# Kernel optimization log

Hardware: AMD Instinct MI355X
Metric: run time of the kernel (lower is better)

The kernel has to match this reference:

```python
import jax, jax.numpy as jnp
import numpy as np

N = 10000      # nodes
E = 320000     # edges (avg degree 32)
H = 64         # hidden_nf
D = 3          # num_dims
L = 4          # n_layers
IN_NODE = 1
IN_EDGE = 2
CEMB = 16      # class_embedding_dim
FH = 32        # field_hidden_size


def setup_inputs() -> dict:
    key = jax.random.key(0)
    ks = iter(jax.random.split(key, 64))
    def nrm(shape, scale=0.05):
        return jax.random.normal(next(ks), shape, dtype=jnp.float32) * scale
    def zeros(shape):
        return jnp.zeros(shape, dtype=jnp.float32)
    inp = {
        # forward args
        "h": nrm((N, IN_NODE), 1.0),
        "x": nrm((N, D), 1.0),
        "vel": nrm((N, D), 1.0),
        "edge_attr": nrm((E, IN_EDGE), 1.0),
        "edges": jax.random.randint(next(ks), (2, E), 0, N, dtype=jnp.int32),
        "charges": jax.random.randint(next(ks), (N,), 0, 2, dtype=jnp.int32),
        # node embedding Linear(in_node_nf, hidden_nf)
        "emb_W": nrm((IN_NODE, H)), "emb_b": zeros((H,)),
        # FieldNetwork: Embedding(2, 16) + MLP(2*D+16 -> 32 -> 32 -> D), SiLU
        "cls_emb": nrm((2, CEMB)),
        "f_W1": nrm((2 * D + CEMB, FH)), "f_b1": zeros((FH,)),
        "f_W2": nrm((FH, FH)), "f_b2": zeros((FH,)),
        "f_W3": nrm((FH, D)), "f_b3": zeros((D,)),
        # per-layer E_GCL_vel_field params, stacked on leading layer dim L
        # edge_mlp: (2H + 1 radial + in_edge_nf) -> H -> H, SiLU after both
        "e_W1": nrm((L, 2 * H + 1 + IN_EDGE, H)), "e_b1": zeros((L, H)),
        "e_W2": nrm((L, H, H)), "e_b2": zeros((L, H)),
        # node_mlp: (H + H) -> H -> H, SiLU only after first
        "n_W1": nrm((L, 2 * H, H)), "n_b1": zeros((L, H)),
        "n_W2": nrm((L, H, H)), "n_b2": zeros((L, H)),
        # coord_mlp: H -> H -> 1 (last layer bias-free, small xavier init)
        "c_W1": nrm((L, H, H)), "c_b1": zeros((L, H)),
        "c_W2": nrm((L, H, 1), 0.001),
        # coord_mlp_vel: H -> H -> 1
        "v_W1": nrm((L, H, H)), "v_b1": zeros((L, H)),
        "v_W2": nrm((L, H, 1)), "v_b2": zeros((L, 1)),
        # coord_mlp_field: H -> H -> 1 (field gating, Aether extension)
        "g_W1": nrm((L, H, H)), "g_b1": zeros((L, H)),
        "g_W2": nrm((L, H, 1)), "g_b2": zeros((L, 1)),
    }
    return inp


def _egnn_forward(h, x, vel, edge_attr, emb_W, emb_b, cls_emb,
                  f_W1, f_b1, f_W2, f_b2, f_W3, f_b3,
                  e_W1, e_b1, e_W2, e_b2, n_W1, n_b1, n_W2, n_b2,
                  c_W1, c_b1, c_W2, v_W1, v_b1, v_W2, v_b2,
                  g_W1, g_b1, g_W2, g_b2, edges, charges):
    row, col = edges[0], edges[1]
    # FieldNetwork: field(pos, vel, charge_class) -> [N, D]
    finp = jnp.concatenate([x, vel, cls_emb[charges]], axis=-1)   # [N, 2D+CEMB]
    fh = jax.nn.silu(finp @ f_W1 + f_b1)
    fh = jax.nn.silu(fh @ f_W2 + f_b2)
    field = fh @ f_W3 + f_b3                                       # [N, D]

    hh = h @ emb_W + emb_b                                         # [N, H]
    coord = x
    ones_e = jnp.ones((E, 1), dtype=x.dtype)
    for i in range(L):
        # coord2radial
        diff = coord[row] - coord[col]                             # [E, D]
        radial = jnp.sum(diff * diff, axis=-1, keepdims=True)      # [E, 1]
        # edge model (gather + MLP)
        e_in = jnp.concatenate([hh[row], hh[col], radial, edge_attr], axis=-1)
        m = jax.nn.silu(e_in @ e_W1[i] + e_b1[i])
        m = jax.nn.silu(m @ e_W2[i] + e_b2[i])                     # [E, H]
        # coord model: mean-aggregate weighted diffs (coords_weight = 1.0)
        cw = jax.nn.silu(m @ c_W1[i] + c_b1[i]) @ c_W2[i]          # [E, 1]
        trans = diff * cw
        csum = jax.ops.segment_sum(trans, row, num_segments=N)     # [N, D]
        cnt = jax.ops.segment_sum(ones_e, row, num_segments=N)     # [N, 1]
        coord = coord + csum / jnp.maximum(cnt, 1.0)
        # velocity and field terms
        vw = jax.nn.silu(hh @ v_W1[i] + v_b1[i]) @ v_W2[i] + v_b2[i]   # [N,1]
        gw = jax.nn.silu(hh @ g_W1[i] + g_b1[i]) @ g_W2[i] + g_b2[i]   # [N,1]
        coord = coord + vw * vel + gw * field
        # node model (scatter-sum messages + MLP)
        magg = jax.ops.segment_sum(m, row, num_segments=N)         # [N, H]
        n_in = jnp.concatenate([hh, magg], axis=-1)
        hh = jax.nn.silu(n_in @ n_W1[i] + n_b1[i]) @ n_W2[i] + n_b2[i]
    return coord


def reference(h, x, vel, edge_attr, edges, charges, emb_W, emb_b, cls_emb,
              f_W1, f_b1, f_W2, f_b2, f_W3, f_b3,
              e_W1, e_b1, e_W2, e_b2, n_W1, n_b1, n_W2, n_b2,
              c_W1, c_b1, c_W2, v_W1, v_b1, v_W2, v_b2,
              g_W1, g_b1, g_W2, g_b2):
    return _egnn_forward(h, x, vel, edge_attr, emb_W, emb_b, cls_emb,
                         f_W1, f_b1, f_W2, f_b2, f_W3, f_b3,
                         e_W1, e_b1, e_W2, e_b2, n_W1, n_b1, n_W2, n_b2,
                         c_W1, c_b1, c_W2, v_W1, v_b1, v_W2, v_b2,
                         g_W1, g_b1, g_W2, g_b2, edges, charges)
```

## Files before the change

kernel.cpp:

```cpp
#include <hip/hip_runtime.h>
#include <hip/hip_bf16.h>

typedef unsigned short ushort_t;
typedef unsigned int uint_t;

#define NN    10000
#define NE    320000
#define NL    4
#define EBLK  64
#define NEBLK 5000
#define NPB   64
#define NNODEBLK 157
#define NPB2  16
#define NODEBLK2 625

#define OFF_FIELD 0
#define OFF_HH    30000
#define OFF_CSUM  670000
#define OFF_MAGG  700000
#define IOFF_CNTI   0
#define IOFF_OFF    10000
#define IOFF_CURSOR 20001
#define IOFF_PERM   30001
#define IOFF_PRER   350004
#define IOFF_PREC   670004
#define IOFF_WCONV  990004
#define WC_EW1  0
#define WC_EW2  4096
#define WC_CW1  6144
#define WC_VW1  8192
#define WC_GW1  10240
#define WC_NW1  12288

__device__ __forceinline__ float silu(float x) {
    return x * __builtin_amdgcn_rcpf(1.0f + __expf(-x));
}

typedef __fp16 half2v __attribute__((ext_vector_type(2)));
typedef __fp16 f16x8 __attribute__((ext_vector_type(8)));
typedef float f32x4 __attribute__((ext_vector_type(4)));
union U4H8 { uint4 u; f16x8 h; };
__device__ __forceinline__ half2v u2h(uint_t u) {
    union { uint_t u; half2v h; } x; x.u = u; return x.h;
}
__device__ __forceinline__ uint_t h2u(half2v h) {
    union { half2v h; uint_t u; } x; x.h = h; return x.u;
}
__device__ __forceinline__ half2v pkrtz(float a, float b) {
    return __builtin_amdgcn_cvt_pkrtz(a, b);
}
__device__ __forceinline__ float dot2h(half2v a, uint_t w, float c) {
#if __has_builtin(__builtin_amdgcn_fdot2)
    return __builtin_amdgcn_fdot2(a, u2h(w), c, false);
#else
    union { uint_t u; __fp16 h[2]; } x; x.u = w;
    return c + (float)a.x * (float)x.h[0] + (float)a.y * (float)x.h[1];
#endif
}
__device__ __forceinline__ ushort_t f2hbits(float f) {
    union { __fp16 h; ushort_t u; } x; x.h = (__fp16)f; return x.u;
}

__global__ __launch_bounds__(256) void wconv_kernel(
    const float* __restrict__ eW1, const float* __restrict__ eW2,
    const float* __restrict__ cW1, const float* __restrict__ vW1,
    const float* __restrict__ gW1, const float* __restrict__ nW1,
    uint_t* __restrict__ out)
{
    const int l = blockIdx.x;
    const int t = threadIdx.x;
    uint_t* o = out + l * 16384;
    const float* e1 = eW1 + l * 8384;
    const float* e2 = eW2 + l * 4096;
    const float* c1 = cW1 + l * 4096;
    const float* v1 = vW1 + l * 4096;
    const float* g1 = gW1 + l * 4096;
    const float* n1 = nW1 + l * 8192;

    for (int i = t; i < 4096; i += 256)
        o[WC_EW1 + i] = h2u(pkrtz(e1[(i >> 6) * 128 + (i & 63)],
                                  e1[(i >> 6) * 128 + 64 + (i & 63)]));
    for (int i = t; i < 2048; i += 256) {
        const int kp = i >> 6, bc = i & 63;
        const uint_t v = h2u(pkrtz(e2[kp * 128 + bc], e2[kp * 128 + 64 + bc]));
        o[WC_EW2 + bc * 32 + (((kp >> 2) ^ (bc & 7)) << 2) + (kp & 3)] = v;
    }
    for (int i = t; i < 2048; i += 256) {
        const int kp = i >> 6, bc = i & 63;
        const uint_t v = h2u(pkrtz(c1[kp * 128 + bc], c1[kp * 128 + 64 + bc]));
        o[WC_CW1 + bc * 32 + (((kp >> 2) ^ (bc & 7)) << 2) + (kp & 3)] = v;
    }
    for (int i = t; i < 2048; i += 256)
        o[WC_VW1 + i] = h2u(pkrtz(v1[(i >> 6) * 128 + (i & 63)],
                                  v1[(i >> 6) * 128 + 64 + (i & 63)]));
    for (int i = t; i < 2048; i += 256)
        o[WC_GW1 + i] = h2u(pkrtz(g1[(i >> 6) * 128 + (i & 63)],
                                  g1[(i >> 6) * 128 + 64 + (i & 63)]));
    for (int i = t; i < 4096; i += 256)
        o[WC_NW1 + i] = h2u(pkrtz(n1[(i >> 6) * 128 + (i & 63)],
                                  n1[(i >> 6) * 128 + 64 + (i & 63)]));
}

__global__ __launch_bounds__(256) void counti_kernel(const int* __restrict__ rows,
                                                     int* __restrict__ cnti) {
    const int e = blockIdx.x * 256 + threadIdx.x;
    if (e < NE) {
        int r = rows[e];
        r = ((uint_t)r < (uint_t)NN) ? r : 0;
        atomicAdd(&cnti[r], 1);
    }
}

__global__ __launch_bounds__(1024) void scan_kernel(const int* __restrict__ cnti,
                                                    int* __restrict__ off,
                                                    int* __restrict__ cursor) {
    __shared__ int part[1024];
    const int t = threadIdx.x;
    const int base = t * 10;
    int loc[10];
    int s = 0;
    #pragma unroll
    for (int i = 0; i < 10; i++) {
        const int idx = base + i;
        const int v = (idx < NN) ? cnti[idx] : 0;
        loc[i] = s; s += v;
    }
    part[t] = s;
    __syncthreads();
    const int own = s;
    for (int d = 1; d < 1024; d <<= 1) {
        const int v = (t >= d) ? part[t - d] : 0;
        __syncthreads();
        part[t] += v;
        __syncthreads();
    }
    const int excl = part[t] - own;
    #pragma unroll
    for (int i = 0; i < 10; i++) {
        const int idx = base + i;
        if (idx < NN) { const int o = excl + loc[i]; off[idx] = o; cursor[idx] = o; }
    }
    if (t == 0) off[NN] = NE;
}

__global__ __launch_bounds__(256) void scatter_kernel(const int* __restrict__ rows,
                                                      int* __restrict__ cursor,
                                                      int* __restrict__ perm) {
    const int e = blockIdx.x * 256 + threadIdx.x;
    if (e < NE) {
        int r = rows[e];
        r = ((uint_t)r < (uint_t)NN) ? r : 0;
        const int pos = atomicAdd(&cursor[r], 1);
        if ((uint_t)pos < (uint_t)NE) perm[pos] = e;
    }
}

__global__ __launch_bounds__(256) void node_init(
    const float* __restrict__ hsrc, const float* __restrict__ xsrc,
    const float* __restrict__ vsrc, const int* __restrict__ charges,
    const float* __restrict__ cls,
    const float* __restrict__ fW1, const float* __restrict__ fb1,
    const float* __restrict__ fW2, const float* __restrict__ fb2,
    const float* __restrict__ fW3, const float* __restrict__ fb3,
    const float* __restrict__ embW, const float* __restrict__ embb,
    float* __restrict__ coord, float* __restrict__ field, float* __restrict__ hh)
{
    __shared__ float sFW1[704], sFW2[1024], sFW3[96];
    __shared__ float sFB1[32], sFB2[32], sFB3[3], sCLS[32], sEW[64], sEB[64];
    const int t = threadIdx.x;
    for (int i = t; i < 704; i += 256) sFW1[i] = fW1[i];
    for (int i = t; i < 1024; i += 256) sFW2[i] = fW2[i];
    if (t < 96) sFW3[t] = fW3[t];
    if (t < 32) { sFB1[t] = fb1[t]; sFB2[t] = fb2[t]; sCLS[t] = cls[t]; }
    if (t < 3)  sFB3[t] = fb3[t];
    if (t < 64) { sEW[t] = embW[t]; sEB[t] = embb[t]; }
    __syncthreads();

    const int n = blockIdx.x * 256 + t;
    if (n >= NN) return;

    float fin[22];
    #pragma unroll
    for (int d = 0; d < 3; d++) {
        fin[d]     = xsrc[3 * n + d];
        fin[3 + d] = vsrc[3 * n + d];
        coord[3 * n + d] = fin[d];
    }
    int ci = charges[n];
    ci = ((uint_t)ci < 2u) ? ci : 0;
    const int cix = ci * 16;
    #pragma unroll
    for (int k = 0; k < 16; k++) fin[6 + k] = sCLS[cix + k];

    float h1[32];
    #pragma unroll
    for (int j = 0; j < 32; j++) h1[j] = sFB1[j];
    #pragma unroll
    for (int k = 0; k < 22; k++) {
        const float v = fin[k];
        #pragma unroll
        for (int j = 0; j < 32; j++) h1[j] += v * sFW1[k * 32 + j];
    }
    #pragma unroll
    for (int j = 0; j < 32; j++) h1[j] = silu(h1[j]);

    float h2[32];
    #pragma unroll
    for (int j = 0; j < 32; j++) h2[j] = sFB2[j];
    #pragma unroll
    for (int k = 0; k < 32; k++) {
        const float v = h1[k];
        #pragma unroll
        for (int j = 0; j < 32; j++) h2[j] += v * sFW2[k * 32 + j];
    }
    #pragma unroll
    for (int j = 0; j < 32; j++) h2[j] = silu(h2[j]);

    #pragma unroll
    for (int d = 0; d < 3; d++) {
        float s = sFB3[d];
        #pragma unroll
        for (int j = 0; j < 32; j++) s += h2[j] * sFW3[j * 3 + d];
        field[3 * n + d] = s;
    }

    const float hv = hsrc[n];
    #pragma unroll
    for (int j = 0; j < 64; j++) hh[(size_t)n * 64 + j] = hv * sEW[j] + sEB[j];
}

__global__ __launch_bounds__(256, 4) void pre_kernel(
    const float* __restrict__ hh,
    const uint_t* __restrict__ w1p, const float* __restrict__ gEB1,
    uint_t* __restrict__ preR, uint_t* __restrict__ preC)
{
    __shared__ __align__(16) uint_t sW1p[4096];
    __shared__ float sB1[64];
    const int t = threadIdx.x;
    for (int i = t; i < 1024; i += 256)
        ((uint4*)sW1p)[i] = ((const uint4*)w1p)[i];
    if (t < 64) sB1[t] = gEB1[t];
    __syncthreads();

    const int ni = t >> 2, q = t & 3;
    int n = blockIdx.x * NPB + ni;
    const bool valid = (n < NN);
    n = valid ? n : (NN - 1);
    const float4* h4p = (const float4*)(hh + (size_t)n * 64);

    float acc[16];
    #pragma unroll
    for (int j = 0; j < 16; j++) acc[j] = sB1[q * 16 + j];
    #pragma unroll
    for (int kk = 0; kk < 16; kk++) {
        const float4 a = h4p[kk];
        const half2v p0 = pkrtz(a.x, a.y);
        const half2v p1 = pkrtz(a.z, a.w);
        const uint4* w0 = (const uint4*)&sW1p[(2 * kk) * 64 + q * 16];
        const uint4* w1 = (const uint4*)&sW1p[(2 * kk + 1) * 64 + q * 16];
        #pragma unroll
        for (int j4 = 0; j4 < 4; j4++) {
            const uint4 wa = w0[j4], wb = w1[j4];
            acc[4*j4+0] = dot2h(p1, wb.x, dot2h(p0, wa.x, acc[4*j4+0]));
            acc[4*j4+1] = dot2h(p1, wb.y, dot2h(p0, wa.y, acc[4*j4+1]));
            acc[4*j4+2] = dot2h(p1, wb.z, dot2h(p0, wa.z, acc[4*j4+2]));
            acc[4*j4+3] = dot2h(p1, wb.w, dot2h(p0, wa.w, acc[4*j4+3]));
        }
    }
    if (valid) {
        uint4 o0, o1;
        o0.x = h2u(pkrtz(acc[0],  acc[1]));  o0.y = h2u(pkrtz(acc[2],  acc[3]));
        o0.z = h2u(pkrtz(acc[4],  acc[5]));  o0.w = h2u(pkrtz(acc[6],  acc[7]));
        o1.x = h2u(pkrtz(acc[8],  acc[9]));  o1.y = h2u(pkrtz(acc[10], acc[11]));
        o1.z = h2u(pkrtz(acc[12], acc[13])); o1.w = h2u(pkrtz(acc[14], acc[15]));
        uint4* dst = (uint4*)(preR + (size_t)n * 32 + q * 8);
        dst[0] = o0; dst[1] = o1;
    }

    #pragma unroll
    for (int j = 0; j < 16; j++) acc[j] = 0.f;
    #pragma unroll
    for (int kk = 0; kk < 16; kk++) {
        const float4 a = h4p[kk];
        const half2v p0 = pkrtz(a.x, a.y);
        const half2v p1 = pkrtz(a.z, a.w);
        const uint4* w0 = (const uint4*)&sW1p[(32 + 2 * kk) * 64 + q * 16];
        const uint4* w1 = (const uint4*)&sW1p[(33 + 2 * kk) * 64 + q * 16];
        #pragma unroll
        for (int j4 = 0; j4 < 4; j4++) {
            const uint4 wa = w0[j4], wb = w1[j4];
            acc[4*j4+0] = dot2h(p1, wb.x, dot2h(p0, wa.x, acc[4*j4+0]));
            acc[4*j4+1] = dot2h(p1, wb.y, dot2h(p0, wa.y, acc[4*j4+1]));
            acc[4*j4+2] = dot2h(p1, wb.z, dot2h(p0, wa.z, acc[4*j4+2]));
            acc[4*j4+3] = dot2h(p1, wb.w, dot2h(p0, wa.w, acc[4*j4+3]));
        }
    }
    if (valid) {
        uint4 o0, o1;
        o0.x = h2u(pkrtz(acc[0],  acc[1]));  o0.y = h2u(pkrtz(acc[2],  acc[3]));
        o0.z = h2u(pkrtz(acc[4],  acc[5]));  o0.w = h2u(pkrtz(acc[6],  acc[7]));
        o1.x = h2u(pkrtz(acc[8],  acc[9]));  o1.y = h2u(pkrtz(acc[10], acc[11]));
        o1.z = h2u(pkrtz(acc[12], acc[13])); o1.w = h2u(pkrtz(acc[14], acc[15]));
        uint4* dst = (uint4*)(preC + (size_t)n * 32 + q * 8);
        dst[0] = o0; dst[1] = o1;
    }
}

__global__ __launch_bounds__(256, 8) void edge_kernel(
    const int* __restrict__ rows, const int* __restrict__ cols,
    const int* __restrict__ perm,
    const float* __restrict__ coord,
    const float* __restrict__ eattr,
    const float* __restrict__ gEW1,
    const uint_t* __restrict__ ewp,
    const float* __restrict__ gEB2,
    const float* __restrict__ gCB1, const float* __restrict__ gCW2,
    const uint_t* __restrict__ preR, const uint_t* __restrict__ preC,
    float* __restrict__ csum, float* __restrict__ magg)
{
    __shared__ __align__(16) uint_t tileh[EBLK * 32];
    __shared__ __align__(16) uint_t sWp[2048];
    __shared__ float sExtW[3 * 64];
    __shared__ float sB2[64], sCB1[64], sCW2v[64];
    __shared__ float scw[EBLK];
    __shared__ int   sr[EBLK], sc[EBLK], se[EBLK];
    __shared__ int   segstart[EBLK + 1];
    __shared__ int   snseg;

    const int t = threadIdx.x;
    const int bid = blockIdx.x;
    const int lb  = (bid & 7) * (NEBLK / 8) + (bid >> 3);

    const uint4 cwr0 = ((const uint4*)(ewp + WC_CW1))[t];
    const uint4 cwr1 = ((const uint4*)(ewp + WC_CW1))[t + 256];

    for (int i = t; i < 512; i += 256)
        ((uint4*)sWp)[i] = ((const uint4*)(ewp + WC_EW2))[i];
    if (t < 192) sExtW[t] = gEW1[8192 + t];
    if (t < 64) { sB2[t] = gEB2[t]; sCB1[t] = gCB1[t]; sCW2v[t] = gCW2[t]; }

    if (t < EBLK) {
        int e = perm[lb * EBLK + t];
        e = ((uint_t)e < (uint_t)NE) ? e : 0;
        int r = rows[e], c = cols[e];
        r = ((uint_t)r < (uint_t)NN) ? r : 0;
        c = ((uint_t)c < (uint_t)NN) ? c : 0;
        se[t] = e; sr[t] = r; sc[t] = c;
    }
    __syncthreads();

    if (t < EBLK) {
        const int flag = (t == 0) ? 1 : ((sr[t] != sr[t - 1]) ? 1 : 0);
        int isc = flag;
        #pragma unroll
        for (int d = 1; d < EBLK; d <<= 1) {
            const int up = __shfl_up(isc, d);
            if (t >= d) isc += up;
        }
        if (flag) segstart[isc - 1] = t;
        if (t == EBLK - 1) { snseg = isc; segstart[isc] = EBLK; }
    }
    __syncthreads();
    const int nseg = snseg;

    const int ei = t >> 2;
    const int q  = t & 3;
    const int e7 = ei & 7;
    const int r = sr[ei], c = sc[ei], e = se[ei];

    const float dx = coord[3 * r + 0] - coord[3 * c + 0];
    const float dy = coord[3 * r + 1] - coord[3 * c + 1];
    const float dz = coord[3 * r + 2] - coord[3 * c + 2];
    const float radial = dx * dx + dy * dy + dz * dz;
    const float2 ea = ((const float2*)eattr)[e];

    union { uint4 v[2]; uint_t a[8]; } R, C;
    {
        const uint4* pr = (const uint4*)(preR + (size_t)r * 32);
        const uint4* pc = (const uint4*)(preC + (size_t)c * 32);
        R.v[0] = pr[q * 2]; R.v[1] = pr[q * 2 + 1];
        C.v[0] = pc[q * 2]; C.v[1] = pc[q * 2 + 1];
    }
    float acc16[16];
    #pragma unroll
    for (int p = 0; p < 8; p++) {
        const half2v hr = u2h(R.a[p]);
        const half2v hc = u2h(C.a[p]);
        acc16[2 * p]     = (float)hr.x + (float)hc.x;
        acc16[2 * p + 1] = (float)hr.y + (float)hc.y;
    }
    {
        const float ext3[3] = {radial, ea.x, ea.y};
        #pragma unroll
        for (int x = 0; x < 3; x++) {
            const float v = ext3[x];
            const float* w = &sExtW[x * 64 + q * 16];
            #pragma unroll
            for (int j = 0; j < 16; j++) acc16[j] += v * w[j];
        }
    }
    #pragma unroll
    for (int j = 0; j < 16; j++) acc16[j] = silu(acc16[j]);
    {
        uint4 g0, g1;
        g0.x = h2u(pkrtz(acc16[0],  acc16[1]));  g0.y = h2u(pkrtz(acc16[2],  acc16[3]));
        g0.z = h2u(pkrtz(acc16[4],  acc16[5]));  g0.w = h2u(pkrtz(acc16[6],  acc16[7]));
        g1.x = h2u(pkrtz(acc16[8],  acc16[9]));  g1.y = h2u(pkrtz(acc16[10], acc16[11]));
        g1.z = h2u(pkrtz(acc16[12], acc16[13])); g1.w = h2u(pkrtz(acc16[14], acc16[15]));
        ((uint4*)tileh)[ei * 8 + ((q * 2) ^ e7)]     = g0;
        ((uint4*)tileh)[ei * 8 + ((q * 2 + 1) ^ e7)] = g1;
    }
    __syncthreads();

    const int lane = t & 63;
    const int wv   = t >> 6;
    const int lrow = lane & 15;
    const int lkg  = lane >> 4;
    const int arow = wv * 16 + lrow;
    const int e7a  = arow & 7;

    U4H8 a0, a1;
    a0.u = ((const uint4*)tileh)[arow * 8 + (lkg ^ e7a)];
    a1.u = ((const uint4*)tileh)[arow * 8 + ((4 + lkg) ^ e7a)];

    f32x4 accn[4];
    #pragma unroll
    for (int n = 0; n < 4; n++) {
        const float b = sB2[n * 16 + lrow];
        f32x4 v = {b, b, b, b};
        accn[n] = v;
    }
    #pragma unroll
    for (int n = 0; n < 4; n++) {
        const int bc = n * 16 + lrow;
        const int b7 = bc & 7;
        U4H8 b0, b1;
        b0.u = ((const uint4*)sWp)[bc * 8 + (lkg ^ b7)];
        b1.u = ((const uint4*)sWp)[bc * 8 + ((4 + lkg) ^ b7)];
        accn[n] = __builtin_amdgcn_mfma_f32_16x16x32_f16(a0.h, b0.h, accn[n], 0, 0, 0);
        accn[n] = __builtin_amdgcn_mfma_f32_16x16x32_f16(a1.h, b1.h, accn[n], 0, 0, 0);
    }
    __syncthreads();

    ((uint4*)sWp)[t]       = cwr0;
    ((uint4*)sWp)[t + 256] = cwr1;
    {
        ushort_t* th16 = (ushort_t*)tileh;
        const int mrow = wv * 16 + lkg * 4;
        #pragma unroll
        for (int n = 0; n < 4; n++) {
            const int ch = n * 16 + lrow;
            const int wi = ch >> 1;
            const int wg = wi >> 2, wj = wi & 3, hl = ch & 1;
            #pragma unroll
            for (int r2 = 0; r2 < 4; r2++) {
                const int edge = mrow + r2;
                th16[(edge * 32 + ((wg ^ (edge & 7)) << 2) + wj) * 2 + hl] =
                    f2hbits(silu(accn[n][r2]));
            }
        }
    }
    __syncthreads();

    U4H8 ma0, ma1;
    ma0.u = ((const uint4*)tileh)[arow * 8 + (lkg ^ e7a)];
    ma1.u = ((const uint4*)tileh)[arow * 8 + ((4 + lkg) ^ e7a)];
    f32x4 cacc[4];
    #pragma unroll
    for (int n = 0; n < 4; n++) {
        const float b = sCB1[n * 16 + lrow];
        f32x4 v = {b, b, b, b};
        cacc[n] = v;
    }
    #pragma unroll
    for (int n = 0; n < 4; n++) {
        const int bc = n * 16 + lrow;
        const int b7 = bc & 7;
        U4H8 b0, b1;
        b0.u = ((const uint4*)sWp)[bc * 8 + (lkg ^ b7)];
        b1.u = ((const uint4*)sWp)[bc * 8 + ((4 + lkg) ^ b7)];
        cacc[n] = __builtin_amdgcn_mfma_f32_16x16x32_f16(ma0.h, b0.h, cacc[n], 0, 0, 0);
        cacc[n] = __builtin_amdgcn_mfma_f32_16x16x32_f16(ma1.h, b1.h, cacc[n], 0, 0, 0);
    }
    float p0 = 0.f, p1 = 0.f, p2 = 0.f, p3 = 0.f;
    #pragma unroll
    for (int n = 0; n < 4; n++) {
        const float w2v = sCW2v[n * 16 + lrow];
        p0 += silu(cacc[n][0]) * w2v;
        p1 += silu(cacc[n][1]) * w2v;
        p2 += silu(cacc[n][2]) * w2v;
        p3 += silu(cacc[n][3]) * w2v;
    }
    #pragma unroll
    for (int m = 1; m <= 8; m <<= 1) {
        p0 += __shfl_xor(p0, m);
        p1 += __shfl_xor(p1, m);
        p2 += __shfl_xor(p2, m);
        p3 += __shfl_xor(p3, m);
    }
    if (lrow == 0) {
        const int mrow = wv * 16 + lkg * 4;
        scw[mrow + 0] = p0; scw[mrow + 1] = p1;
        scw[mrow + 2] = p2; scw[mrow + 3] = p3;
    }

    for (int w = t; w < nseg * 64; w += 256) {
        const int lr2 = w >> 6, cc = w & 63;
        const int pp0 = segstart[lr2], pp1 = segstart[lr2 + 1];
        const int kp = cc >> 1, hi = cc & 1;
        const int kg = kp >> 2, kj = kp & 3;
        float s = 0.f;
        for (int p = pp0; p < pp1; p++) {
            const half2v h = u2h(tileh[p * 32 + ((kg ^ (p & 7)) << 2) + kj]);
            s += hi ? (float)h.y : (float)h.x;
        }
        atomicAdd(&magg[(size_t)sr[pp0] * 64 + cc], s);
    }
    __syncthreads();

    const float cw = scw[ei];
    float* tf = (float*)tileh;
    if (q < 3) tf[ei * 4 + q] = (q == 0 ? dx : (q == 1 ? dy : dz)) * cw;
    __syncthreads();
    for (int w = t; w < nseg * 3; w += 256) {
        const int lr2 = w / 3, cc = w - 3 * lr2;
        const int pp0 = segstart[lr2], pp1 = segstart[lr2 + 1];
        float s = 0.f;
        for (int p = pp0; p < pp1; p++) s += tf[p * 4 + cc];
        atomicAdd(&csum[3 * sr[pp0] + cc], s);
    }
}

__global__ __launch_bounds__(256, 2) void node_kernel(
    const uint_t* __restrict__ nwp,
    const uint_t* __restrict__ nwpn,
    const float* __restrict__ gVB1, const float* __restrict__ gVW2,
    const float* __restrict__ gVB2,
    const float* __restrict__ gGB1, const float* __restrict__ gGW2,
    const float* __restrict__ gGB2,
    const float* __restrict__ gNB1,
    const float* __restrict__ gNW2, const float* __restrict__ gNB2,
    const float* __restrict__ gB1n,
    float* __restrict__ csum, const int* __restrict__ off,
    const float* __restrict__ vsrc, const float* __restrict__ field,
    float* __restrict__ magg,
    float* __restrict__ coord, float* __restrict__ hh,
    uint_t* __restrict__ preR, uint_t* __restrict__ preC, const int emit_pre)
{
    __shared__ __align__(16) uint_t sNW1p[4096];
    __shared__ __align__(16) uint_t sW1np[4096];
    __shared__ __align__(16) uint_t sVW1p[2048];
    __shared__ __align__(16) uint_t sGW1p[2048];
    __shared__ __align__(16) float sNW2[4096];
    __shared__ __align__(16) float tile[NPB2 * 136];
    __shared__ float sNB1[64], sNB2[64], sB1n[64];

    const int t = threadIdx.x;
    for (int i = t; i < 1024; i += 256)
        ((uint4*)sNW1p)[i] = ((const uint4*)(nwp + WC_NW1))[i];
    for (int i = t; i < 1024; i += 256)
        ((uint4*)sW1np)[i] = ((const uint4*)(nwpn + WC_EW1))[i];
    for (int i = t; i < 512; i += 256)
        ((uint4*)sVW1p)[i] = ((const uint4*)(nwp + WC_VW1))[i];
    for (int i = t; i < 512; i += 256)
        ((uint4*)sGW1p)[i] = ((const uint4*)(nwp + WC_GW1))[i];
    for (int i = t; i < 1024; i += 256)
        ((float4*)sNW2)[i] = ((const float4*)gNW2)[i];
    if (t < 64) { sNB1[t] = gNB1[t]; sNB2[t] = gNB2[t]; sB1n[t] = gB1n[t]; }

    const int ni = t >> 4;
    const int q  = t & 15;
    const int n = blockIdx.x * NPB2 + ni;
    float* T = &tile[ni * 136];

    ((float4*)T)[q]        = ((const float4*)(hh + (size_t)n * 64))[q];
    ((float4*)(T + 68))[q] = ((const float4*)(magg + (size_t)n * 64))[q];
    __syncthreads();

    float v4[4], g4[4];
    {
        const float4 bv = ((const float4*)gVB1)[q];
        const float4 bg = ((const float4*)gGB1)[q];
        v4[0] = bv.x; v4[1] = bv.y; v4[2] = bv.z; v4[3] = bv.w;
        g4[0] = bg.x; g4[1] = bg.y; g4[2] = bg.z; g4[3] = bg.w;
    }
    #pragma unroll 8
    for (int kp = 0; kp < 32; kp++) {
        const half2v p = pkrtz(T[2 * kp], T[2 * kp + 1]);
        const uint4 wv = *(const uint4*)&sVW1p[kp * 64 + q * 4];
        const uint4 wg = *(const uint4*)&sGW1p[kp * 64 + q * 4];
        v4[0] = dot2h(p, wv.x, v4[0]); v4[1] = dot2h(p, wv.y, v4[1]);
        v4[2] = dot2h(p, wv.z, v4[2]); v4[3] = dot2h(p, wv.w, v4[3]);
        g4[0] = dot2h(p, wg.x, g4[0]); g4[1] = dot2h(p, wg.y, g4[1]);
        g4[2] = dot2h(p, wg.z, g4[2]); g4[3] = dot2h(p, wg.w, g4[3]);
    }
    float partv, partg;
    {
        const float4 wv2 = ((const float4*)gVW2)[q];
        const float4 wg2 = ((const float4*)gGW2)[q];
        partv = silu(v4[0]) * wv2.x + silu(v4[1]) * wv2.y
              + silu(v4[2]) * wv2.z + silu(v4[3]) * wv2.w;
        partg = silu(g4[0]) * wg2.x + silu(g4[1]) * wg2.y
              + silu(g4[2]) * wg2.z + silu(g4[3]) * wg2.w;
    }
    partv += __shfl_xor(partv, 1);  partg += __shfl_xor(partg, 1);
    partv += __shfl_xor(partv, 2);  partg += __shfl_xor(partg, 2);
    partv += __shfl_xor(partv, 4);  partg += __shfl_xor(partg, 4);
    partv += __shfl_xor(partv, 8);  partg += __shfl_xor(partg, 8);
    const float vw = partv + gVB2[0];
    const float gw = partg + gGB2[0];

    if (q == 0) {
        const float cn = fmaxf((float)(off[n + 1] - off[n]), 1.0f);
        #pragma unroll
        for (int d = 0; d < 3; d++)
            coord[3 * n + d] += csum[3 * n + d] / cn
                              + vw * vsrc[3 * n + d]
                              + gw * field[3 * n + d];
    }

    float aA[4], aB[4];
    {
        const float4 b = ((const float4*)sNB1)[q];
        aA[0] = b.x; aA[1] = b.y; aA[2] = b.z; aA[3] = b.w;
        aB[0] = aB[1] = aB[2] = aB[3] = 0.f;
    }
    #pragma unroll 8
    for (int kp = 0; kp < 32; kp++) {
        const half2v pA = pkrtz(T[2 * kp], T[2 * kp + 1]);
        const half2v pB = pkrtz(T[68 + 2 * kp], T[68 + 2 * kp + 1]);
        const uint4 wA = *(const uint4*)&sNW1p[kp * 64 + q * 4];
        const uint4 wB = *(const uint4*)&sNW1p[(32 + kp) * 64 + q * 4];
        aA[0] = dot2h(pA, wA.x, aA[0]); aA[1] = dot2h(pA, wA.y, aA[1]);
        aA[2] = dot2h(pA, wA.z, aA[2]); aA[3] = dot2h(pA, wA.w, aA[3]);
        aB[0] = dot2h(pB, wB.x, aB[0]); aB[1] = dot2h(pB, wB.y, aB[1]);
        aB[2] = dot2h(pB, wB.z, aB[2]); aB[3] = dot2h(pB, wB.w, aB[3]);
    }
    float a4[4];
    #pragma unroll
    for (int j = 0; j < 4; j++) a4[j] = silu(aA[j] + aB[j]);

    __syncthreads();
    {
        float4 v; v.x = a4[0]; v.y = a4[1]; v.z = a4[2]; v.w = a4[3];
        ((float4*)T)[q] = v;
    }
    __syncthreads();

    {
        float4 z; z.x = z.y = z.z = z.w = 0.f;
        ((float4*)(magg + (size_t)n * 64))[q] = z;
        if (q == 0) { csum[3 * n] = 0.f; csum[3 * n + 1] = 0.f; csum[3 * n + 2] = 0.f; }
    }

    float oA[4], oB[4];
    {
        const float4 b = ((const float4*)sNB2)[q];
        oA[0] = b.x; oA[1] = b.y; oA[2] = b.z; oA[3] = b.w;
        oB[0] = oB[1] = oB[2] = oB[3] = 0.f;
    }
    #pragma unroll 4
    for (int kk = 0; kk < 8; kk++) {
        const float4 hA = ((const float4*)T)[2 * kk];
        const float4 hB = ((const float4*)T)[2 * kk + 1];
        const float avA[4] = {hA.x, hA.y, hA.z, hA.w};
        const float avB[4] = {hB.x, hB.y, hB.z, hB.w};
        #pragma unroll
        for (int u = 0; u < 4; u++) {
            const float vA = avA[u];
            const float vB = avB[u];
            const float4 wA = ((const float4*)(sNW2 + (8 * kk + u) * 64))[q];
            const float4 wB = ((const float4*)(sNW2 + (8 * kk + 4 + u) * 64))[q];
            oA[0] += vA * wA.x; oA[1] += vA * wA.y; oA[2] += vA * wA.z; oA[3] += vA * wA.w;
            oB[0] += vB * wB.x; oB[1] += vB * wB.y; oB[2] += vB * wB.z; oB[3] += vB * wB.w;
        }
    }
    float o4[4];
    #pragma unroll
    for (int j = 0; j < 4; j++) o4[j] = oA[j] + oB[j];
    {
        float4 v; v.x = o4[0]; v.y = o4[1]; v.z = o4[2]; v.w = o4[3];
        ((float4*)(hh + (size_t)n * 64))[q] = v;
    }

    if (emit_pre) {
        __syncthreads();
        {
            float4 v; v.x = o4[0]; v.y = o4[1]; v.z = o4[2]; v.w = o4[3];
            ((float4*)T)[q] = v;
        }
        __syncthreads();

        float aR[4], aC[4];
        {
            const float4 b = ((const float4*)sB1n)[q];
            aR[0] = b.x; aR[1] = b.y; aR[2] = b.z; aR[3] = b.w;
            aC[0] = aC[1] = aC[2] = aC[3] = 0.f;
        }
        #pragma unroll 8
        for (int kp = 0; kp < 32; kp++) {
            const half2v p = pkrtz(T[2 * kp], T[2 * kp + 1]);
            const uint4 wr = *(const uint4*)&sW1np[kp * 64 + q * 4];
            const uint4 wc = *(const uint4*)&sW1np[(32 + kp) * 64 + q * 4];
            aR[0] = dot2h(p, wr.x, aR[0]); aR[1] = dot2h(p, wr.y, aR[1]);
            aR[2] = dot2h(p, wr.z, aR[2]); aR[3] = dot2h(p, wr.w, aR[3]);
            aC[0] = dot2h(p, wc.x, aC[0]); aC[1] = dot2h(p, wc.y, aC[1]);
            aC[2] = dot2h(p, wc.z, aC[2]); aC[3] = dot2h(p, wc.w, aC[3]);
        }
        uint2 oR, oC;
        oR.x = h2u(pkrtz(aR[0], aR[1])); oR.y = h2u(pkrtz(aR[2], aR[3]));
        oC.x = h2u(pkrtz(aC[0], aC[1])); oC.y = h2u(pkrtz(aC[2], aC[3]));
        *(uint2*)(preR + (size_t)n * 32 + q * 2) = oR;
        *(uint2*)(preC + (size_t)n * 32 + q * 2) = oC;
    }
}

extern "C" void kernel_launch(void* const* d_in, const int* in_sizes, int n_in,
                              void* d_out, int out_size, void* d_ws, size_t ws_size,
                              hipStream_t stream) {
    float* wsf = (float*)d_ws;
    int*   wsi = (int*)(wsf + 1340000);
    uint_t* preR  = (uint_t*)(wsi + IOFF_PRER);
    uint_t* preC  = (uint_t*)(wsi + IOFF_PREC);
    uint_t* wconv = (uint_t*)(wsi + IOFF_WCONV);
    float* coord = (float*)d_out;
    const int* edges = (const int*)d_in[4];
    const int* rows = edges;
    const int* cols = edges + NE;

    hipMemsetAsync(wsi + IOFF_CNTI, 0, NN * sizeof(int), stream);
    wconv_kernel<<<NL, 256, 0, stream>>>(
        (const float*)d_in[15], (const float*)d_in[17], (const float*)d_in[23],
        (const float*)d_in[26], (const float*)d_in[30], (const float*)d_in[19],
        wconv);
    counti_kernel<<<(NE + 255) / 256, 256, 0, stream>>>(rows, wsi + IOFF_CNTI);
    scan_kernel<<<1, 1024, 0, stream>>>(wsi + IOFF_CNTI, wsi + IOFF_OFF, wsi + IOFF_CURSOR);
    scatter_kernel<<<(NE + 255) / 256, 256, 0, stream>>>(rows, wsi + IOFF_CURSOR,
                                                         wsi + IOFF_PERM);

    node_init<<<(NN + 255) / 256, 256, 0, stream>>>(
        (const float*)d_in[0], (const float*)d_in[1], (const float*)d_in[2],
        (const int*)d_in[5], (const float*)d_in[8],
        (const float*)d_in[9],  (const float*)d_in[10],
        (const float*)d_in[11], (const float*)d_in[12],
        (const float*)d_in[13], (const float*)d_in[14],
        (const float*)d_in[6],  (const float*)d_in[7],
        coord, wsf + OFF_FIELD, wsf + OFF_HH);

    hipMemsetAsync(wsf + OFF_CSUM, 0, (30000 + 640000) * sizeof(float), stream);

    pre_kernel<<<NNODEBLK, 256, 0, stream>>>(
        wsf + OFF_HH,
        wconv + 0 * 16384 + WC_EW1, (const float*)d_in[16],
        preR, preC);

    for (int l = 0; l < NL; l++) {
        const int ln = (l + 1 < NL) ? (l + 1) : 0;
        edge_kernel<<<NEBLK, 256, 0, stream>>>(
            rows, cols, wsi + IOFF_PERM,
            coord, (const float*)d_in[3],
            ((const float*)d_in[15]) + l * 8384,
            wconv + l * 16384,
            ((const float*)d_in[18]) + l * 64,
            ((const float*)d_in[24]) + l * 64,
            ((const float*)d_in[25]) + l * 64,
            preR, preC,
            wsf + OFF_CSUM, wsf + OFF_MAGG);
        node_kernel<<<NODEBLK2, 256, 0, stream>>>(
            wconv + l * 16384, wconv + ln * 16384,
            ((const float*)d_in[27]) + l * 64,
            ((const float*)d_in[28]) + l * 64,   ((const float*)d_in[29]) + l,
            ((const float*)d_in[31]) + l * 64,
            ((const float*)d_in[32]) + l * 64,   ((const float*)d_in[33]) + l,
            ((const float*)d_in[20]) + l * 64,
            ((const float*)d_in[21]) + l * 4096, ((const float*)d_in[22]) + l * 64,
            ((const float*)d_in[16]) + ln * 64,
            wsf + OFF_CSUM, wsi + IOFF_OFF, (const float*)d_in[2],
            wsf + OFF_FIELD, wsf + OFF_MAGG, coord, wsf + OFF_HH,
            preR, preC, (l + 1 < NL) ? 1 : 0);
    }
}
```

Baseline: 465.7 us.

## Move node_kernel matmuls onto MFMA with swizzled fp16 weight layouts

Rewrites node_kernel so the velocity/field gating, node MLP layers and next-layer pre-projection run as 16x16x32 fp16 MFMA instructions instead of per-thread dot2 and fp32 FMA loops. The weight-conversion kernel now emits XOR-swizzled, channel-major fp16 copies of these weights, including the node second layer, which was previously fp32. Node tiles are staged in LDS as fp16. This reduces ALU work and LDS footprint in the node phase, at the cost of fp16 precision in the second node layer and a larger workspace per layer.

```diff
diff --git a/kernel.cpp b/kernel.cpp
--- a/kernel.cpp
+++ b/kernel.cpp
@@ -25,12 +25,14 @@
 #define IOFF_PRER   350004
 #define IOFF_PREC   670004
 #define IOFF_WCONV  990004
-#define WC_EW1  0
-#define WC_EW2  4096
-#define WC_CW1  6144
-#define WC_VW1  8192
-#define WC_GW1  10240
-#define WC_NW1  12288
+#define WC_EW1   0
+#define WC_EW2   4096
+#define WC_CW1   6144
+#define WC_VG    8192
+#define WC_NW1S  12288
+#define WC_NW2S  16384
+#define WC_EW1S  18432
+#define WC_SIZE  22528
 
 __device__ __forceinline__ float silu(float x) {
     return x * __builtin_amdgcn_rcpf(1.0f + __expf(-x));
@@ -65,17 +67,19 @@
     const float* __restrict__ eW1, const float* __restrict__ eW2,
     const float* __restrict__ cW1, const float* __restrict__ vW1,
     const float* __restrict__ gW1, const float* __restrict__ nW1,
+    const float* __restrict__ nW2,
     uint_t* __restrict__ out)
 {
     const int l = blockIdx.x;
     const int t = threadIdx.x;
-    uint_t* o = out + l * 16384;
+    uint_t* o = out + l * WC_SIZE;
     const float* e1 = eW1 + l * 8384;
     const float* e2 = eW2 + l * 4096;
     const float* c1 = cW1 + l * 4096;
     const float* v1 = vW1 + l * 4096;
     const float* g1 = gW1 + l * 4096;
     const float* n1 = nW1 + l * 8192;
+    const float* n2 = nW2 + l * 4096;
 
     for (int i = t; i < 4096; i += 256)
         o[WC_EW1 + i] = h2u(pkrtz(e1[(i >> 6) * 128 + (i & 63)],
@@ -90,15 +94,37 @@
         const uint_t v = h2u(pkrtz(c1[kp * 128 + bc], c1[kp * 128 + 64 + bc]));
         o[WC_CW1 + bc * 32 + (((kp >> 2) ^ (bc & 7)) << 2) + (kp & 3)] = v;
     }
-    for (int i = t; i < 2048; i += 256)
-        o[WC_VW1 + i] = h2u(pkrtz(v1[(i >> 6) * 128 + (i & 63)],
-                                  v1[(i >> 6) * 128 + 64 + (i & 63)]));
-    for (int i = t; i < 2048; i += 256)
-        o[WC_GW1 + i] = h2u(pkrtz(g1[(i >> 6) * 128 + (i & 63)],
-                                  g1[(i >> 6) * 128 + 64 + (i & 63)]));
-    for (int i = t; i < 4096; i += 256)
-        o[WC_NW1 + i] = h2u(pkrtz(n1[(i >> 6) * 128 + (i & 63)],
-                                  n1[(i >> 6) * 128 + 64 + (i & 63)]));
+    for (int i = t; i < 2048; i += 256) {
+        const int kp = i >> 6, ch = i & 63;
+        const uint_t v = h2u(pkrtz(v1[kp * 128 + ch], v1[kp * 128 + 64 + ch]));
+        o[WC_VG + ch * 32 + (((kp >> 2) ^ (ch & 7)) << 2) + (kp & 3)] = v;
+    }
+    for (int i = t; i < 2048; i += 256) {
+        const int kp = i >> 6, ch = i & 63;
+        const uint_t v = h2u(pkrtz(g1[kp * 128 + ch], g1[kp * 128 + 64 + ch]));
+        o[WC_VG + (64 + ch) * 32 + (((kp >> 2) ^ (ch & 7)) << 2) + (kp & 3)] = v;
+    }
+    for (int i = t; i < 4096; i += 256) {
+        const int kp = i >> 6, ch = i & 63;
+        const uint_t v = h2u(pkrtz(n1[kp * 128 + ch], n1[kp * 128 + 64 + ch]));
+        o[WC_NW1S + ch * 64 + (((kp >> 2) ^ (ch & 15)) << 2) + (kp & 3)] = v;
+    }
+    for (int i = t; i < 2048; i += 256) {
+        const int kp = i >> 6, ch = i & 63;
+        const uint_t v = h2u(pkrtz(n2[kp * 128 + ch], n2[kp * 128 + 64 + ch]));
+        o[WC_NW2S + ch * 32 + (((kp >> 2) ^ (ch & 7)) << 2) + (kp & 3)] = v;
+    }
+    for (int i = t; i < 2048; i += 256) {
+        const int kp = i >> 6, ch = i & 63;
+        const uint_t v = h2u(pkrtz(e1[kp * 128 + ch], e1[kp * 128 + 64 + ch]));
+        o[WC_EW1S + ch * 32 + (((kp >> 2) ^ (ch & 7)) << 2) + (kp & 3)] = v;
+    }
+    for (int i = t; i < 2048; i += 256) {
+        const int kp = i >> 6, ch = i & 63;
+        const uint_t v = h2u(pkrtz(e1[(64 + 2 * kp) * 64 + ch],
+                                   e1[(64 + 2 * kp + 1) * 64 + ch]));
+        o[WC_EW1S + (64 + ch) * 32 + (((kp >> 2) ^ (ch & 7)) << 2) + (kp & 3)] = v;
+    }
 }
 
 __global__ __launch_bounds__(256) void counti_kernel(const int* __restrict__ rows,
@@ -532,14 +558,12 @@
 }
 
 __global__ __launch_bounds__(256, 2) void node_kernel(
-    const uint_t* __restrict__ nwp,
-    const uint_t* __restrict__ nwpn,
+    const uint_t* __restrict__ nwp, const uint_t* __restrict__ nwpn,
     const float* __restrict__ gVB1, const float* __restrict__ gVW2,
     const float* __restrict__ gVB2,
     const float* __restrict__ gGB1, const float* __restrict__ gGW2,
     const float* __restrict__ gGB2,
-    const float* __restrict__ gNB1,
-    const float* __restrict__ gNW2, const float* __restrict__ gNB2,
+    const float* __restrict__ gNB1, const float* __restrict__ gNB2,
     const float* __restrict__ gB1n,
     float* __restrict__ csum, const int* __restrict__ off,
     const float* __restrict__ vsrc, const float* __restrict__ field,
@@ -547,171 +571,179 @@
     float* __restrict__ coord, float* __restrict__ hh,
     uint_t* __restrict__ preR, uint_t* __restrict__ preC, const int emit_pre)
 {
-    __shared__ __align__(16) uint_t sNW1p[4096];
-    __shared__ __align__(16) uint_t sW1np[4096];
-    __shared__ __align__(16) uint_t sVW1p[2048];
-    __shared__ __align__(16) uint_t sGW1p[2048];
-    __shared__ __align__(16) float sNW2[4096];
-    __shared__ __align__(16) float tile[NPB2 * 136];
+    __shared__ __align__(16) uint_t sVG[4096];
+    __shared__ __align__(16) uint_t sNW1S[4096];
+    __shared__ __align__(16) uint_t sNW2S[2048];
+    __shared__ __align__(16) uint_t sW1nS[4096];
+    __shared__ __align__(16) uint_t tileA[1024];
+    __shared__ __align__(16) uint_t tileM[512];
+    __shared__ float pV[64], pG[64];
+    __shared__ float sVB1[64], sGB1[64], sVW2[64], sGW2[64];
     __shared__ float sNB1[64], sNB2[64], sB1n[64];
 
     const int t = threadIdx.x;
-    for (int i = t; i < 1024; i += 256)
-        ((uint4*)sNW1p)[i] = ((const uint4*)(nwp + WC_NW1))[i];
-    for (int i = t; i < 1024; i += 256)
-        ((uint4*)sW1np)[i] = ((const uint4*)(nwpn + WC_EW1))[i];
-    for (int i = t; i < 512; i += 256)
-        ((uint4*)sVW1p)[i] = ((const uint4*)(nwp + WC_VW1))[i];
-    for (int i = t; i < 512; i += 256)
-        ((uint4*)sGW1p)[i] = ((const uint4*)(nwp + WC_GW1))[i];
-    for (int i = t; i < 1024; i += 256)
-        ((float4*)sNW2)[i] = ((const float4*)gNW2)[i];
-    if (t < 64) { sNB1[t] = gNB1[t]; sNB2[t] = gNB2[t]; sB1n[t] = gB1n[t]; }
-
-    const int ni = t >> 4;
-    const int q  = t & 15;
-    const int n = blockIdx.x * NPB2 + ni;
-    float* T = &tile[ni * 136];
-
-    ((float4*)T)[q]        = ((const float4*)(hh + (size_t)n * 64))[q];
-    ((float4*)(T + 68))[q] = ((const float4*)(magg + (size_t)n * 64))[q];
-    __syncthreads();
-
-    float v4[4], g4[4];
-    {
-        const float4 bv = ((const float4*)gVB1)[q];
-        const float4 bg = ((const float4*)gGB1)[q];
-        v4[0] = bv.x; v4[1] = bv.y; v4[2] = bv.z; v4[3] = bv.w;
-        g4[0] = bg.x; g4[1] = bg.y; g4[2] = bg.z; g4[3] = bg.w;
-    }
-    #pragma unroll 8
-    for (int kp = 0; kp < 32; kp++) {
-        const half2v p = pkrtz(T[2 * kp], T[2 * kp + 1]);
-        const uint4 wv = *(const uint4*)&sVW1p[kp * 64 + q * 4];
-        const uint4 wg = *(const uint4*)&sGW1p[kp * 64 + q * 4];
-        v4[0] = dot2h(p, wv.x, v4[0]); v4[1] = dot2h(p, wv.y, v4[1]);
-        v4[2] = dot2h(p, wv.z, v4[2]); v4[3] = dot2h(p, wv.w, v4[3]);
-        g4[0] = dot2h(p, wg.x, g4[0]); g4[1] = dot2h(p, wg.y, g4[1]);
-        g4[2] = dot2h(p, wg.z, g4[2]); g4[3] = dot2h(p, wg.w, g4[3]);
-    }
-    float partv, partg;
-    {
-        const float4 wv2 = ((const float4*)gVW2)[q];
-        const float4 wg2 = ((const float4*)gGW2)[q];
-        partv = silu(v4[0]) * wv2.x + silu(v4[1]) * wv2.y
-              + silu(v4[2]) * wv2.z + silu(v4[3]) * wv2.w;
-        partg = silu(g4[0]) * wg2.x + silu(g4[1]) * wg2.y
-              + silu(g4[2]) * wg2.z + silu(g4[3]) * wg2.w;
-    }
-    partv += __shfl_xor(partv, 1);  partg += __shfl_xor(partg, 1);
-    partv += __shfl_xor(partv, 2);  partg += __shfl_xor(partg, 2);
-    partv += __shfl_xor(partv, 4);  partg += __shfl_xor(partg, 4);
-    partv += __shfl_xor(partv, 8);  partg += __shfl_xor(partg, 8);
-    const float vw = partv + gVB2[0];
-    const float gw = partg + gGB2[0];
+    for (int i = t; i < 1024; i += 256) ((uint4*)sVG)[i]   = ((const uint4*)(nwp + WC_VG))[i];
+    for (int i = t; i < 1024; i += 256) ((uint4*)sNW1S)[i] = ((const uint4*)(nwp + WC_NW1S))[i];
+    for (int i = t; i < 512;  i += 256) ((uint4*)sNW2S)[i] = ((const uint4*)(nwp + WC_NW2S))[i];
+    for (int i = t; i < 1024; i += 256) ((uint4*)sW1nS)[i] = ((const uint4*)(nwpn + WC_EW1S))[i];
+    if (t < 64) { sVB1[t] = gVB1[t]; sGB1[t] = gGB1[t];
+                  sVW2[t] = gVW2[t]; sGW2[t] = gGW2[t];
+                  sNB1[t] = gNB1[t]; sNB2[t] = gNB2[t]; sB1n[t] = gB1n[t]; }
+
+    const int ni = t >> 4, q = t & 15;
+    const int nb = blockIdx.x * NPB2;
+    const int n  = nb + ni;
+
+    {
+        const float4* src = (q < 8) ? (const float4*)(hh + (size_t)n * 64)
+                                    : (const float4*)(magg + (size_t)n * 64);
+        const int qq = q & 7;
+        const float4 f0 = src[2 * qq], f1 = src[2 * qq + 1];
+        uint4 u;
+        u.x = h2u(pkrtz(f0.x, f0.y)); u.y = h2u(pkrtz(f0.z, f0.w));
+        u.z = h2u(pkrtz(f1.x, f1.y)); u.w = h2u(pkrtz(f1.z, f1.w));
+        ((uint4*)tileA)[ni * 16 + (q ^ ni)] = u;
+    }
+    __syncthreads();
+
+    const int lane = t & 63, wv = t >> 6;
+    const int lrow = lane & 15, lkg = lane >> 4;
+    const int ch = wv * 16 + lrow;
+    const int ch7 = ch & 7, ch15 = ch & 15;
+
+    U4H8 aA0, aA1, aA2, aA3;
+    aA0.u = ((const uint4*)tileA)[lrow * 16 + ((0 + lkg) ^ lrow)];
+    aA1.u = ((const uint4*)tileA)[lrow * 16 + ((4 + lkg) ^ lrow)];
+    aA2.u = ((const uint4*)tileA)[lrow * 16 + ((8 + lkg) ^ lrow)];
+    aA3.u = ((const uint4*)tileA)[lrow * 16 + ((12 + lkg) ^ lrow)];
+
+    f32x4 accV, accG;
+    { const float b = sVB1[ch]; f32x4 v = {b, b, b, b}; accV = v; }
+    { const float b = sGB1[ch]; f32x4 v = {b, b, b, b}; accG = v; }
+    {
+        U4H8 bv0, bv1, bg0, bg1;
+        bv0.u = ((const uint4*)sVG)[ch * 8 + (lkg ^ ch7)];
+        bv1.u = ((const uint4*)sVG)[ch * 8 + ((4 + lkg) ^ ch7)];
+        bg0.u = ((const uint4*)sVG)[(64 + ch) * 8 + (lkg ^ ch7)];
+        bg1.u = ((const uint4*)sVG)[(64 + ch) * 8 + ((4 + lkg) ^ ch7)];
+        accV = __builtin_amdgcn_mfma_f32_16x16x32_f16(aA0.h, bv0.h, accV, 0, 0, 0);
+        accV = __builtin_amdgcn_mfma_f32_16x16x32_f16(aA1.h, bv1.h, accV, 0, 0, 0);
+        accG = __builtin_amdgcn_mfma_f32_16x16x32_f16(aA0.h, bg0.h, accG, 0, 0, 0);
+        accG = __builtin_amdgcn_mfma_f32_16x16x32_f16(aA1.h, bg1.h, accG, 0, 0, 0);
+    }
+    {
+        float pv0 = silu(accV[0]) * sVW2[ch], pv1 = silu(accV[1]) * sVW2[ch];
+        float pv2 = silu(accV[2]) * sVW2[ch], pv3 = silu(accV[3]) * sVW2[ch];
+        float pg0 = silu(accG[0]) * sGW2[ch], pg1 = silu(accG[1]) * sGW2[ch];
+        float pg2 = silu(accG[2]) * sGW2[ch], pg3 = silu(accG[3]) * sGW2[ch];
+        #pragma unroll
+        for (int m = 1; m <= 8; m <<= 1) {
+            pv0 += __shfl_xor(pv0, m); pv1 += __shfl_xor(pv1, m);
+            pv2 += __shfl_xor(pv2, m); pv3 += __shfl_xor(pv3, m);
+            pg0 += __shfl_xor(pg0, m); pg1 += __shfl_xor(pg1, m);
+            pg2 += __shfl_xor(pg2, m); pg3 += __shfl_xor(pg3, m);
+        }
+        if (lrow == 0) {
+            const int base = wv * 16 + lkg * 4;
+            pV[base + 0] = pv0; pV[base + 1] = pv1;
+            pV[base + 2] = pv2; pV[base + 3] = pv3;
+            pG[base + 0] = pg0; pG[base + 1] = pg1;
+            pG[base + 2] = pg2; pG[base + 3] = pg3;
+        }
+    }
+
+    f32x4 accH;
+    { const float b = sNB1[ch]; f32x4 v = {b, b, b, b}; accH = v; }
+    {
+        U4H8 w0, w1, w2, w3;
+        w0.u = ((const uint4*)sNW1S)[ch * 16 + ((0 + lkg) ^ ch15)];
+        w1.u = ((const uint4*)sNW1S)[ch * 16 + ((4 + lkg) ^ ch15)];
+        w2.u = ((const uint4*)sNW1S)[ch * 16 + ((8 + lkg) ^ ch15)];
+        w3.u = ((const uint4*)sNW1S)[ch * 16 + ((12 + lkg) ^ ch15)];
+        accH = __builtin_amdgcn_mfma_f32_16x16x32_f16(aA0.h, w0.h, accH, 0, 0, 0);
+        accH = __builtin_amdgcn_mfma_f32_16x16x32_f16(aA1.h, w1.h, accH, 0, 0, 0);
+        accH = __builtin_amdgcn_mfma_f32_16x16x32_f16(aA2.h, w2.h, accH, 0, 0, 0);
+        accH = __builtin_amdgcn_mfma_f32_16x16x32_f16(aA3.h, w3.h, accH, 0, 0, 0);
+    }
+    {
+        ushort_t* tm16 = (ushort_t*)tileM;
+        const int wi = ch >> 1;
+        const int wg = wi >> 2, wj = wi & 3, hl = ch & 1;
+        #pragma unroll
+        for (int r2 = 0; r2 < 4; r2++) {
+            const int node = lkg * 4 + r2;
+            tm16[(node * 32 + ((wg ^ (node & 7)) << 2) + wj) * 2 + hl] =
+                f2hbits(silu(accH[r2]));
+        }
+    }
+    __syncthreads();
 
     if (q == 0) {
+        const float vw = gVB2[0] + pV[ni] + pV[16 + ni] + pV[32 + ni] + pV[48 + ni];
+        const float gw = gGB2[0] + pG[ni] + pG[16 + ni] + pG[32 + ni] + pG[48 + ni];
         const float cn = fmaxf((float)(off[n + 1] - off[n]), 1.0f);
         #pragma unroll
         for (int d = 0; d < 3; d++)
             coord[3 * n + d] += csum[3 * n + d] / cn
                               + vw * vsrc[3 * n + d]
                               + gw * field[3 * n + d];
-    }
-
-    float aA[4], aB[4];
-    {
-        const float4 b = ((const float4*)sNB1)[q];
-        aA[0] = b.x; aA[1] = b.y; aA[2] = b.z; aA[3] = b.w;
-        aB[0] = aB[1] = aB[2] = aB[3] = 0.f;
-    }
-    #pragma unroll 8
-    for (int kp = 0; kp < 32; kp++) {
-        const half2v pA = pkrtz(T[2 * kp], T[2 * kp + 1]);
-        const half2v pB = pkrtz(T[68 + 2 * kp], T[68 + 2 * kp + 1]);
-        const uint4 wA = *(const uint4*)&sNW1p[kp * 64 + q * 4];
-        const uint4 wB = *(const uint4*)&sNW1p[(32 + kp) * 64 + q * 4];
-        aA[0] = dot2h(pA, wA.x, aA[0]); aA[1] = dot2h(pA, wA.y, aA[1]);
-        aA[2] = dot2h(pA, wA.z, aA[2]); aA[3] = dot2h(pA, wA.w, aA[3]);
-        aB[0] = dot2h(pB, wB.x, aB[0]); aB[1] = dot2h(pB, wB.y, aB[1]);
-        aB[2] = dot2h(pB, wB.z, aB[2]); aB[3] = dot2h(pB, wB.w, aB[3]);
-    }
-    float a4[4];
-    #pragma unroll
-    for (int j = 0; j < 4; j++) a4[j] = silu(aA[j] + aB[j]);
-
-    __syncthreads();
-    {
-        float4 v; v.x = a4[0]; v.y = a4[1]; v.z = a4[2]; v.w = a4[3];
-        ((float4*)T)[q] = v;
-    }
-    __syncthreads();
-
+        csum[3 * n] = 0.f; csum[3 * n + 1] = 0.f; csum[3 * n + 2] = 0.f;
+    }
     {
         float4 z; z.x = z.y = z.z = z.w = 0.f;
         ((float4*)(magg + (size_t)n * 64))[q] = z;
-        if (q == 0) { csum[3 * n] = 0.f; csum[3 * n + 1] = 0.f; csum[3 * n + 2] = 0.f; }
-    }
-
-    float oA[4], oB[4];
-    {
-        const float4 b = ((const float4*)sNB2)[q];
-        oA[0] = b.x; oA[1] = b.y; oA[2] = b.z; oA[3] = b.w;
-        oB[0] = oB[1] = oB[2] = oB[3] = 0.f;
-    }
-    #pragma unroll 4
-    for (int kk = 0; kk < 8; kk++) {
-        const float4 hA = ((const float4*)T)[2 * kk];
-        const float4 hB = ((const float4*)T)[2 * kk + 1];
-        const float avA[4] = {hA.x, hA.y, hA.z, hA.w};
-        const float avB[4] = {hB.x, hB.y, hB.z, hB.w};
-        #pragma unroll
-        for (int u = 0; u < 4; u++) {
-            const float vA = avA[u];
-            const float vB = avB[u];
-            const float4 wA = ((const float4*)(sNW2 + (8 * kk + u) * 64))[q];
-            const float4 wB = ((const float4*)(sNW2 + (8 * kk + 4 + u) * 64))[q];
-            oA[0] += vA * wA.x; oA[1] += vA * wA.y; oA[2] += vA * wA.z; oA[3] += vA * wA.w;
-            oB[0] += vB * wB.x; oB[1] += vB * wB.y; oB[2] += vB * wB.z; oB[3] += vB * wB.w;
-        }
-    }
-    float o4[4];
-    #pragma unroll
-    for (int j = 0; j < 4; j++) o4[j] = oA[j] + oB[j];
-    {
-        float4 v; v.x = o4[0]; v.y = o4[1]; v.z = o4[2]; v.w = o4[3];
-        ((float4*)(hh + (size_t)n * 64))[q] = v;
-    }
+    }
+
+    f32x4 accO;
+    { const float b = sNB2[ch]; f32x4 v = {b, b, b, b}; accO = v; }
+    {
+        U4H8 m0, m1, w0, w1;
+        m0.u = ((const uint4*)tileM)[lrow * 8 + (lkg ^ (lrow & 7))];
+        m1.u = ((const uint4*)tileM)[lrow * 8 + ((4 + lkg) ^ (lrow & 7))];
+        w0.u = ((const uint4*)sNW2S)[ch * 8 + (lkg ^ ch7)];
+        w1.u = ((const uint4*)sNW2S)[ch * 8 + ((4 + lkg) ^ ch7)];
+        accO = __builtin_amdgcn_mfma_f32_16x16x32_f16(m0.h, w0.h, accO, 0, 0, 0);
+        accO = __builtin_amdgcn_mfma_f32_16x16x32_f16(m1.h, w1.h, accO, 0, 0, 0);
+    }
+    #pragma unroll
+    for (int r2 = 0; r2 < 4; r2++)
+        hh[(size_t)(nb + lkg * 4 + r2) * 64 + ch] = accO[r2];
 
     if (emit_pre) {
+        {
+            ushort_t* ta16 = (ushort_t*)tileA;
+            const int wi = ch >> 1;
+            const int wg = wi >> 2, wj = wi & 3, hl = ch & 1;
+            #pragma unroll
+            for (int r2 = 0; r2 < 4; r2++) {
+                const int node = lkg * 4 + r2;
+                ta16[(node * 64 + ((wg ^ (node & 15)) << 2) + wj) * 2 + hl] =
+                    f2hbits(accO[r2]);
+            }
+        }
         __syncthreads();
-        {
-            float4 v; v.x = o4[0]; v.y = o4[1]; v.z = o4[2]; v.w = o4[3];
-            ((float4*)T)[q] = v;
-        }
-        __syncthreads();
-
-        float aR[4], aC[4];
-        {
-            const float4 b = ((const float4*)sB1n)[q];
-            aR[0] = b.x; aR[1] = b.y; aR[2] = b.z; aR[3] = b.w;
-            aC[0] = aC[1] = aC[2] = aC[3] = 0.f;
-        }
-        #pragma unroll 8
-        for (int kp = 0; kp < 32; kp++) {
-            const half2v p = pkrtz(T[2 * kp], T[2 * kp + 1]);
-            const uint4 wr = *(const uint4*)&sW1np[kp * 64 + q * 4];
-            const uint4 wc = *(const uint4*)&sW1np[(32 + kp) * 64 + q * 4];
-            aR[0] = dot2h(p, wr.x, aR[0]); aR[1] = dot2h(p, wr.y, aR[1]);
-            aR[2] = dot2h(p, wr.z, aR[2]); aR[3] = dot2h(p, wr.w, aR[3]);
-            aC[0] = dot2h(p, wc.x, aC[0]); aC[1] = dot2h(p, wc.y, aC[1]);
-            aC[2] = dot2h(p, wc.z, aC[2]); aC[3] = dot2h(p, wc.w, aC[3]);
-        }
-        uint2 oR, oC;
-        oR.x = h2u(pkrtz(aR[0], aR[1])); oR.y = h2u(pkrtz(aR[2], aR[3]));
-        oC.x = h2u(pkrtz(aC[0], aC[1])); oC.y = h2u(pkrtz(aC[2], aC[3]));
-        *(uint2*)(preR + (size_t)n * 32 + q * 2) = oR;
-        *(uint2*)(preC + (size_t)n * 32 + q * 2) = oC;
+        U4H8 h0, h1, wr0, wr1, wc0, wc1;
+        h0.u = ((const uint4*)tileA)[lrow * 16 + ((0 + lkg) ^ lrow)];
+        h1.u = ((const uint4*)tileA)[lrow * 16 + ((4 + lkg) ^ lrow)];
+        wr0.u = ((const uint4*)sW1nS)[ch * 8 + (lkg ^ ch7)];
+        wr1.u = ((const uint4*)sW1nS)[ch * 8 + ((4 + lkg) ^ ch7)];
+        wc0.u = ((const uint4*)sW1nS)[(64 + ch) * 8 + (lkg ^ ch7)];
+        wc1.u = ((const uint4*)sW1nS)[(64 + ch) * 8 + ((4 + lkg) ^ ch7)];
+        f32x4 accR, accC;
+        { const float b = sB1n[ch]; f32x4 v = {b, b, b, b}; accR = v; }
+        { f32x4 v = {0.f, 0.f, 0.f, 0.f}; accC = v; }
+        accR = __builtin_amdgcn_mfma_f32_16x16x32_f16(h0.h, wr0.h, accR, 0, 0, 0);
+        accR = __builtin_amdgcn_mfma_f32_16x16x32_f16(h1.h, wr1.h, accR, 0, 0, 0);
+        accC = __builtin_amdgcn_mfma_f32_16x16x32_f16(h0.h, wc0.h, accC, 0, 0, 0);
+        accC = __builtin_amdgcn_mfma_f32_16x16x32_f16(h1.h, wc1.h, accC, 0, 0, 0);
+        ushort_t* pRu = (ushort_t*)preR;
+        ushort_t* pCu = (ushort_t*)preC;
+        #pragma unroll
+        for (int r2 = 0; r2 < 4; r2++) {
+            const size_t g = (size_t)(nb + lkg * 4 + r2) * 64 + ch;
+            pRu[g] = f2hbits(accR[r2]);
+            pCu[g] = f2hbits(accC[r2]);
+        }
     }
 }
 
@@ -732,6 +764,7 @@
     wconv_kernel<<<NL, 256, 0, stream>>>(
         (const float*)d_in[15], (const float*)d_in[17], (const float*)d_in[23],
         (const float*)d_in[26], (const float*)d_in[30], (const float*)d_in[19],
+        (const float*)d_in[21],
         wconv);
     counti_kernel<<<(NE + 255) / 256, 256, 0, stream>>>(rows, wsi + IOFF_CNTI);
     scan_kernel<<<1, 1024, 0, stream>>>(wsi + IOFF_CNTI, wsi + IOFF_OFF, wsi + IOFF_CURSOR);
@@ -751,7 +784,7 @@
 
     pre_kernel<<<NNODEBLK, 256, 0, stream>>>(
         wsf + OFF_HH,
-        wconv + 0 * 16384 + WC_EW1, (const float*)d_in[16],
+        wconv + 0 * WC_SIZE + WC_EW1, (const float*)d_in[16],
         preR, preC);
 
     for (int l = 0; l < NL; l++) {
@@ -760,20 +793,19 @@
             rows, cols, wsi + IOFF_PERM,
             coord, (const float*)d_in[3],
             ((const float*)d_in[15]) + l * 8384,
-            wconv + l * 16384,
+            wconv + l * WC_SIZE,
             ((const float*)d_in[18]) + l * 64,
             ((const float*)d_in[24]) + l * 64,
             ((const float*)d_in[25]) + l * 64,
             preR, preC,
             wsf + OFF_CSUM, wsf + OFF_MAGG);
         node_kernel<<<NODEBLK2, 256, 0, stream>>>(
-            wconv + l * 16384, wconv + ln * 16384,
+            wconv + l * WC_SIZE, wconv + ln * WC_SIZE,
             ((const float*)d_in[27]) + l * 64,
             ((const float*)d_in[28]) + l * 64,   ((const float*)d_in[29]) + l,
             ((const float*)d_in[31]) + l * 64,
             ((const float*)d_in[32]) + l * 64,   ((const float*)d_in[33]) + l,
-            ((const float*)d_in[20]) + l * 64,
-            ((const float*)d_in[21]) + l * 4096, ((const float*)d_in[22]) + l * 64,
+            ((const float*)d_in[20]) + l * 64,   ((const float*)d_in[22]) + l * 64,
             ((const float*)d_in[16]) + ln * 64,
             wsf + OFF_CSUM, wsi + IOFF_OFF, (const float*)d_in[2],
             wsf + OFF_FIELD, wsf + OFF_MAGG, coord, wsf + OFF_HH,
```

Measured after the change: 441.0 us. -5.3%, faster.
